# Kernel tuning notes

Hardware: AMD Instinct MI355X
Metric: run time of the kernel (lower is better)

## Reference

```python
import jax, jax.numpy as jnp
import numpy as np

T1, T2, T3 = 0.05, 0.1, 0.15
EPS = 1e-8  # matches torch cosine_similarity clamp


def _propagate(x, t):
    # GEmbedding: cosine-similarity adjacency  [B,N,F] -> [B,N,N]
    xn = x / jnp.maximum(jnp.linalg.norm(x, axis=-1, keepdims=True), EPS)
    adj = jnp.einsum('bnf,bmf->bnm', xn, xn)
    # F.threshold(adj, t, 0): keep values strictly greater than t
    adj = jnp.where(adj > t, adj, 0.0)
    # GraphAdjNorm: D^{-1/2} A D^{-1/2} via row/col broadcast (same math as
    # the original diag-matmul, without materializing diagonal matrices)
    d = jnp.sum(adj, axis=-1)              # [B,N]
    inv_sqrt = 1.0 / jnp.sqrt(d)           # [B,N]
    adj = adj * inv_sqrt[..., :, None] * inv_sqrt[..., None, :]
    return jnp.einsum('bnm,bmf->bnf', adj, x)


def setup_inputs() -> dict:
    key = jax.random.key(0)
    k1, k2 = jax.random.split(key)
    B, N, F = 8, 2048, 128
    x = jax.random.normal(k1, (B, N, F), dtype=jnp.float32)
    weight = jax.random.normal(k2, (F, F), dtype=jnp.float32) * 0.05
    return {"x": x, "weight": weight}


def reference(x, weight):
    res = x
    h = x
    for t in (T1, T2, T3):
        h = _propagate(h, t)
    h = jax.lax.stop_gradient(h)  # torch.no_grad() block
    return jnp.einsum('bnf,fo->bno', h + res, weight)
```

## Files before the change

### kernel.cpp

```cpp
#include <hip/hip_runtime.h>
#include <hip/hip_bf16.h>
#include <cstdint>

#define BQ 8
#define NQ 2048
#define FQ 128
#define NG (NQ * 16)
#define HSS 256.0f

typedef __attribute__((ext_vector_type(8))) short short8;
typedef __attribute__((ext_vector_type(4))) float f32x4;
typedef __attribute__((ext_vector_type(8))) unsigned short us8;
typedef __attribute__((ext_vector_type(2))) unsigned int u32x2;
typedef __attribute__((ext_vector_type(4))) unsigned int u32x4;

__device__ __forceinline__ unsigned short f2bf(float f) {
    union { float f; unsigned int u; } c; c.f = f;
    unsigned int u = c.u;
    u = (u + 0x7FFFu + ((u >> 16) & 1u)) >> 16;
    return (unsigned short)u;
}
__device__ __forceinline__ float bf2f(unsigned short u) {
    union { unsigned int i; float f; } c; c.i = (unsigned int)u << 16; return c.f;
}
__device__ __forceinline__ unsigned int pk8lo(float a, float b, unsigned int old) {
    return (unsigned int)__builtin_amdgcn_cvt_pk_fp8_f32(a, b, (int)old, false);
}
__device__ __forceinline__ unsigned int pk8hi(float a, float b, unsigned int old) {
    return (unsigned int)__builtin_amdgcn_cvt_pk_fp8_f32(a, b, (int)old, true);
}


__global__ __launch_bounds__(256) void k_rownorm(const float* __restrict__ h,
                                                 unsigned short* __restrict__ xnF) {
    int t = threadIdx.x;
    int rl = t >> 4, j = t & 15;
    size_t row = (size_t)blockIdx.x * 16 + rl;
    const float* hr = h + row * FQ + j * 8;
    float v[8];
    #pragma unroll
    for (int e = 0; e < 8; ++e) v[e] = hr[e];
    float s = 0.f;
    #pragma unroll
    for (int e = 0; e < 8; ++e) s += v[e] * v[e];
    s += __shfl_xor(s, 1, 64);
    s += __shfl_xor(s, 2, 64);
    s += __shfl_xor(s, 4, 64);
    s += __shfl_xor(s, 8, 64);
    float inv = 1.0f / fmaxf(sqrtf(s), 1e-8f);
    us8 u;
    #pragma unroll
    for (int e = 0; e < 8; ++e) u[e] = f2bf(v[e] * inv);
    *(us8*)(xnF + (size_t)blockIdx.x * 2048 + j * 128 + rl * 8) = u;
}

__global__ __launch_bounds__(512) void k_adj(const unsigned short* __restrict__ xnF,
                                             unsigned char* __restrict__ adjF,
                                             float* __restrict__ dpart, float t) {
    __shared__ unsigned short As[16384];
    __shared__ union { unsigned short Bsh[16384];
                       unsigned char  T2[128 * 132]; } ub;
    __shared__ float dsm[2][128];
    __shared__ float csm[2][128];

    int bid = blockIdx.x;
    int bb = bid & 7;
    int pr = bid >> 3;
    int I = 0;
    { int p = pr; while (p >= 16 - I) { p -= 16 - I; ++I; } pr = p; }
    int J = I + pr;

    int tid = threadIdx.x;
    int wid = tid >> 6, lane = tid & 63;
    int wr = wid >> 1, wc = wid & 1;
    int g = lane >> 4, c = lane & 15;

    const unsigned short* xb = xnF + (size_t)bb * NQ * FQ;
    int rowb = I * 128 + wr * 32;
    int colb = J * 128 + wc * 64;

    {
        const unsigned short* srcA = xb + (size_t)(I * 8) * 2048;
        const unsigned short* srcB = xb + (size_t)(J * 8) * 2048;
        #pragma unroll
        for (int it = 0; it < 4; ++it) {
            __builtin_amdgcn_global_load_lds(
                (const __attribute__((address_space(1))) void*)(srcA + (size_t)(it * 512 + tid) * 8),
                (__attribute__((address_space(3))) void*)(As + (it * 512 + wid * 64) * 8),
                16, 0, 0);
            __builtin_amdgcn_global_load_lds(
                (const __attribute__((address_space(1))) void*)(srcB + (size_t)(it * 512 + tid) * 8),
                (__attribute__((address_space(3))) void*)(ub.Bsh + (it * 512 + wid * 64) * 8),
                16, 0, 0);
        }
    }
    __syncthreads();

    short8 a[2][4];
    #pragma unroll
    for (int mi = 0; mi < 2; ++mi)
        #pragma unroll
        for (int ks = 0; ks < 4; ++ks)
            a[mi][ks] = *(const short8*)(As + (wr * 2 + mi) * 2048 + (ks * 4 + g) * 128 + c * 8);

    f32x4 acc[2][4];
    #pragma unroll
    for (int mi = 0; mi < 2; ++mi)
        #pragma unroll
        for (int ni = 0; ni < 4; ++ni) acc[mi][ni] = (f32x4){0.f, 0.f, 0.f, 0.f};

    #pragma unroll
    for (int ni = 0; ni < 4; ++ni) {
        short8 b[4];
        #pragma unroll
        for (int ks = 0; ks < 4; ++ks)
            b[ks] = *(const short8*)(ub.Bsh + (wc * 4 + ni) * 2048 + (ks * 4 + g) * 128 + c * 8);
        #pragma unroll
        for (int mi = 0; mi < 2; ++mi)
            #pragma unroll
            for (int ks = 0; ks < 4; ++ks)
                acc[mi][ni] = __builtin_amdgcn_mfma_f32_16x16x32_bf16(a[mi][ks], b[ks], acc[mi][ni], 0, 0, 0);
    }

    __syncthreads();

    unsigned char* adjb = adjF + (size_t)bb * NQ * NQ;
    float dl[2][4];
    float csl[4] = {0.f, 0.f, 0.f, 0.f};
    #pragma unroll
    for (int mi = 0; mi < 2; ++mi)
        #pragma unroll
        for (int r = 0; r < 4; ++r) dl[mi][r] = 0.f;

    #pragma unroll
    for (int mi = 0; mi < 2; ++mi)
        #pragma unroll
        for (int ni = 0; ni < 4; ++ni) {
            f32x4 v = acc[mi][ni];
            float x0 = (v[0] > t) ? v[0] : 0.0f;
            float x1 = (v[1] > t) ? v[1] : 0.0f;
            float x2 = (v[2] > t) ? v[2] : 0.0f;
            float x3 = (v[3] > t) ? v[3] : 0.0f;
            dl[mi][0] += x0; dl[mi][1] += x1; dl[mi][2] += x2; dl[mi][3] += x3;
            csl[ni] += x0 + x1 + x2 + x3;
            unsigned int u = pk8lo(x0, x1, 0u);
            u = pk8hi(x2, x3, u);
            *(unsigned int*)(adjb + (size_t)((colb >> 4) + ni) * NG
                                  + (size_t)((rowb >> 3) + mi * 2 + (g >> 1)) * 128
                                  + c * 8 + (g & 1) * 4) = u;
            if (I != J) {
                int colL = wc * 64 + ni * 16 + c;
                int rowL = wr * 32 + mi * 16 + g * 4;
                *(unsigned int*)(ub.T2 + colL * 132 + rowL) = u;
            }
        }

    #pragma unroll
    for (int mi = 0; mi < 2; ++mi)
        #pragma unroll
        for (int r = 0; r < 4; ++r) {
            float s = dl[mi][r];
            s += __shfl_xor(s, 1, 64);
            s += __shfl_xor(s, 2, 64);
            s += __shfl_xor(s, 4, 64);
            s += __shfl_xor(s, 8, 64);
            dl[mi][r] = s;
        }
    if (c == 0) {
        #pragma unroll
        for (int mi = 0; mi < 2; ++mi)
            #pragma unroll
            for (int r = 0; r < 4; ++r)
                dsm[wc][wr * 32 + mi * 16 + g * 4 + r] = dl[mi][r];
    }
    if (I != J) {
        #pragma unroll
        for (int ni = 0; ni < 4; ++ni) {
            float s = csl[ni];
            s += __shfl_xor(s, 16, 64);
            s += __shfl_xor(s, 32, 64);
            csl[ni] = s;
        }
        if (lane < 16) {
            #pragma unroll
            for (int ni = 0; ni < 4; ++ni)
                csm[wr & 1][wc * 64 + ni * 16 + lane] = csl[ni];
        }
    }
    __syncthreads();
    if (I != J && (wr >= 2) && lane < 16) {
        #pragma unroll
        for (int ni = 0; ni < 4; ++ni)
            csm[wr & 1][wc * 64 + ni * 16 + lane] += csl[ni];
    }
    __syncthreads();

    if (tid < 128)
        dpart[((size_t)J * 8 + bb) * NQ + I * 128 + tid] = dsm[0][tid] + dsm[1][tid];
    if (I != J) {
        if (tid < 128)
            dpart[((size_t)I * 8 + bb) * NQ + J * 128 + tid] = csm[0][tid] + csm[1][tid];
        int ng = wid;
        int mg = lane >> 2;
        int part = lane & 3;
        unsigned int w[8];
        #pragma unroll
        for (int ml = 0; ml < 8; ++ml)
            w[ml] = *(const unsigned int*)(ub.T2 + (mg * 8 + ml) * 132 + ng * 16 + part * 4);
        unsigned int o32[8];
        #pragma unroll
        for (int i = 0; i < 4; ++i)
            #pragma unroll
            for (int h = 0; h < 2; ++h)
                o32[i * 2 + h] = ((w[h * 4 + 0] >> (8 * i)) & 0xFFu)
                               | (((w[h * 4 + 1] >> (8 * i)) & 0xFFu) << 8)
                               | (((w[h * 4 + 2] >> (8 * i)) & 0xFFu) << 16)
                               | (((w[h * 4 + 3] >> (8 * i)) & 0xFFu) << 24);
        unsigned char* dst = adjb + (size_t)(I * 8 + ng) * NG + (size_t)(J * 16 + mg) * 128 + part * 32;
        *(u32x4*)dst        = (u32x4){o32[0], o32[1], o32[2], o32[3]};
        *(u32x4*)(dst + 16) = (u32x4){o32[4], o32[5], o32[6], o32[7]};
    }
}

__global__ __launch_bounds__(256) void k_prep_f32(const float* __restrict__ h,
                                                  const float* __restrict__ dpart,
                                                  float* __restrict__ isq,
                                                  unsigned char* __restrict__ hsF) {
    __shared__ float tile[32][129];
    __shared__ float iv[32];
    int r0 = blockIdx.x * 32;
    int bb = r0 >> 11;
    int m0 = r0 & (NQ - 1);
    int tid = threadIdx.x;
    if (tid < 32) {
        float s = 0.f;
        #pragma unroll
        for (int j = 0; j < 16; ++j)
            s += dpart[((size_t)j * 8 + bb) * NQ + m0 + tid];
        float v = 1.0f / sqrtf(s);
        iv[tid] = v;
        isq[r0 + tid] = v;
    }
    #pragma unroll
    for (int it = 0; it < 16; ++it) {
        int idx = tid + it * 256;
        int mi = idx >> 7, f = idx & 127;
        tile[mi][f] = h[(size_t)(r0 + mi) * FQ + f];
    }
    __syncthreads();
    unsigned char* hb = hsF + (size_t)bb * NQ * FQ;
    #pragma unroll
    for (int it = 0; it < 2; ++it) {
        int p = tid + it * 256;
        int f = p & 127, mc = p >> 7;
        float sv[8];
        #pragma unroll
        for (int e = 0; e < 8; ++e)
            sv[e] = tile[mc * 8 + e][f] * iv[mc * 8 + e] * HSS;
        u32x2 u;
        u[0] = pk8hi(sv[2], sv[3], pk8lo(sv[0], sv[1], 0u));
        u[1] = pk8hi(sv[6], sv[7], pk8lo(sv[4], sv[5], 0u));
        *(u32x2*)(hb + (size_t)((m0 >> 3) + mc) * 1024 + f * 8) = u;
    }
}

__global__ __launch_bounds__(256) void k_prep_bf16(const unsigned short* __restrict__ h,
                                                   const float* __restrict__ dpart,
                                                   float* __restrict__ isq,
                                                   unsigned char* __restrict__ hsF) {
    __shared__ float tile[32][129];
    __shared__ float iv[32];
    int r0 = blockIdx.x * 32;
    int bb = r0 >> 11;
    int m0 = r0 & (NQ - 1);
    int tid = threadIdx.x;
    if (tid < 32) {
        float s = 0.f;
        #pragma unroll
        for (int j = 0; j < 16; ++j)
            s += dpart[((size_t)j * 8 + bb) * NQ + m0 + tid];
        float v = 1.0f / sqrtf(s);
        iv[tid] = v;
        isq[r0 + tid] = v;
    }
    #pragma unroll
    for (int it = 0; it < 16; ++it) {
        int idx = tid + it * 256;
        int mi = idx >> 7, f = idx & 127;
        tile[mi][f] = bf2f(h[(size_t)(r0 + mi) * FQ + f]);
    }
    __syncthreads();
    unsigned char* hb = hsF + (size_t)bb * NQ * FQ;
    #pragma unroll
    for (int it = 0; it < 2; ++it) {
        int p = tid + it * 256;
        int f = p & 127, mc = p >> 7;
        float sv[8];
        #pragma unroll
        for (int e = 0; e < 8; ++e)
            sv[e] = tile[mc * 8 + e][f] * iv[mc * 8 + e] * HSS;
        u32x2 u;
        u[0] = pk8hi(sv[2], sv[3], pk8lo(sv[0], sv[1], 0u));
        u[1] = pk8hi(sv[6], sv[7], pk8lo(sv[4], sv[5], 0u));
        *(u32x2*)(hb + (size_t)((m0 >> 3) + mc) * 1024 + f * 8) = u;
    }
}

template<bool LAST>
__global__ __launch_bounds__(512) void k_gemm3(const unsigned char* __restrict__ adjF,
                                               const unsigned char* __restrict__ hsF,
                                               const float* __restrict__ isq,
                                               unsigned short* __restrict__ hout,
                                               unsigned short* __restrict__ xnF) {
    __shared__ unsigned char Bs[32768];
    __shared__ float red[32][128];

    int bid = blockIdx.x;
    int lb = (bid & 7) * 64 + (bid >> 3);
    int bb = lb >> 6;
    int rt = lb & 63;
    int row0g = rt * 32;
    int tid = threadIdx.x;
    int wid = tid >> 6, lane = tid & 63;
    int g = lane >> 4, c = lane & 15;
    int rg = wid >> 2, kh = wid & 3;
    int wrow = row0g + rg * 16;

    const unsigned char* adjr = adjF + (size_t)bb * NQ * NQ + (size_t)(wrow >> 4) * NG;
    const unsigned char* hb   = hsF + (size_t)bb * NQ * FQ;

    f32x4 acc[8];
    #pragma unroll
    for (int i = 0; i < 8; ++i) acc[i] = (f32x4){0.f, 0.f, 0.f, 0.f};

    int khr = wid >> 1;
    int wlo = wid & 1;

    for (int ph = 0; ph < 8; ++ph) {
        __syncthreads();
        {
            const unsigned char* src = hb + (size_t)(khr * 64 + ph * 8) * 1024 + wlo * 1024;
            unsigned char* dst = Bs + khr * 8192 + wlo * 1024;
            #pragma unroll
            for (int it = 0; it < 4; ++it) {
                __builtin_amdgcn_global_load_lds(
                    (const __attribute__((address_space(1))) void*)(src + it * 2048 + lane * 16),
                    (__attribute__((address_space(3))) void*)(dst + it * 2048),
                    16, 0, 0);
            }
        }
        __syncthreads();
        #pragma unroll
        for (int kk2 = 0; kk2 < 2; ++kk2) {
            int mstep = kh * 16 + ph * 2 + kk2;
            long a0 = *(const long*)(adjr + (size_t)(mstep * 4 + g) * 128 + c * 8);
            #pragma unroll
            for (int ct = 0; ct < 8; ++ct) {
                long bfr = *(const long*)(Bs + kh * 8192 + kk2 * 4096 + g * 1024 + (ct * 16 + c) * 8);
                acc[ct] = __builtin_amdgcn_mfma_f32_16x16x32_fp8_fp8(a0, bfr, acc[ct], 0, 0, 0);
            }
        }
    }

    __syncthreads();
    #pragma unroll
    for (int s = 0; s < 4; ++s) {
        if (kh == s) {
            #pragma unroll
            for (int ct = 0; ct < 8; ++ct)
                #pragma unroll
                for (int r = 0; r < 4; ++r) {
                    int rl = rg * 16 + g * 4 + r;
                    if (s == 0) red[rl][ct * 16 + c] = acc[ct][r];
                    else        red[rl][ct * 16 + c] += acc[ct][r];
                }
        }
        __syncthreads();
    }

    int rl = tid >> 4;
    int j  = tid & 15;
    int n  = row0g + rl;
    float scale = isq[(size_t)bb * NQ + n] * (1.0f / HSS);
    float v[8];
    float s = 0.f;
    #pragma unroll
    for (int e = 0; e < 8; ++e) {
        float x = red[rl][j * 8 + e] * scale;
        v[e] = x;
        s += x * x;
    }
    s += __shfl_xor(s, 1, 64);
    s += __shfl_xor(s, 2, 64);
    s += __shfl_xor(s, 4, 64);
    s += __shfl_xor(s, 8, 64);
    float inv = 1.0f / fmaxf(sqrtf(s), 1e-8f);

    us8 h0;
    #pragma unroll
    for (int e = 0; e < 8; ++e) h0[e] = f2bf(v[e]);
    *(us8*)(hout + ((size_t)bb * NQ + n) * FQ + j * 8) = h0;

    if constexpr (!LAST) {
        us8 u0;
        #pragma unroll
        for (int e = 0; e < 8; ++e) u0[e] = f2bf(v[e] * inv);
        unsigned short* xd = xnF + (size_t)bb * NQ * FQ + (size_t)(n >> 4) * 2048
                                 + j * 128 + (n & 15) * 8;
        *(us8*)xd = u0;
    }
}

__global__ __launch_bounds__(256) void k_out(const unsigned short* __restrict__ h3,
                                             const float* __restrict__ x,
                                             const float* __restrict__ W,
                                             float* __restrict__ out) {
    __shared__ float hx[8][128];
    int r0 = blockIdx.x * 8;
    int tid = threadIdx.x;
    #pragma unroll
    for (int it = 0; it < 4; ++it) {
        int idx = tid + it * 256;
        int ri = idx >> 7, f = idx & 127;
        size_t gi = (size_t)(r0 + ri) * FQ + f;
        hx[ri][f] = bf2f(h3[gi]) + x[gi];
    }
    __syncthreads();
    int o = tid & 127, half = tid >> 7;
    float acc[4] = {0.f, 0.f, 0.f, 0.f};
    for (int f = 0; f < 128; ++f) {
        float wv = W[f * 128 + o];
        #pragma unroll
        for (int j = 0; j < 4; ++j)
            acc[j] += hx[half * 4 + j][f] * wv;
    }
    #pragma unroll
    for (int j = 0; j < 4; ++j)
        out[(size_t)(r0 + half * 4 + j) * FQ + o] = acc[j];
}

extern "C" void kernel_launch(void* const* d_in, const int* in_sizes, int n_in,
                              void* d_out, int out_size, void* d_ws, size_t ws_size,
                              hipStream_t stream) {
    const float* x = (const float*)d_in[0];
    const float* W = (const float*)d_in[1];
    float* out = (float*)d_out;
    char* ws = (char*)d_ws;

    const size_t CS   = (size_t)BQ * NQ * FQ;
    const size_t oADJ = 0;
    const size_t oXN  = oADJ + (size_t)BQ * NQ * NQ;
    const size_t oHST = oXN  + CS * 2;
    const size_t oD   = oHST + CS;
    const size_t oISQ = oD   + (size_t)16 * BQ * NQ * 4;
    const size_t oHA  = oISQ + (size_t)BQ * NQ * 4;
    const size_t oHB  = oHA  + CS * 2;
    const size_t need = oHB  + CS * 2;
    if (ws_size < need) return;

    unsigned char*  adjF = (unsigned char*)(ws + oADJ);
    unsigned short* xnF  = (unsigned short*)(ws + oXN);
    unsigned char*  hsF  = (unsigned char*)(ws + oHST);
    float* dpart = (float*)(ws + oD);
    float* isq   = (float*)(ws + oISQ);
    unsigned short* hA = (unsigned short*)(ws + oHA);
    unsigned short* hB = (unsigned short*)(ws + oHB);

    const float ts[3] = {0.05f, 0.1f, 0.15f};

    k_rownorm<<<BQ * NQ / 16, 256, 0, stream>>>(x, xnF);
    k_adj<<<BQ * 136, 512, 0, stream>>>(xnF, adjF, dpart, ts[0]);
    k_prep_f32<<<BQ * NQ / 32, 256, 0, stream>>>(x, dpart, isq, hsF);
    k_gemm3<false><<<BQ * 64, 512, 0, stream>>>(adjF, hsF, isq, hA, xnF);
    k_adj<<<BQ * 136, 512, 0, stream>>>(xnF, adjF, dpart, ts[1]);
    k_prep_bf16<<<BQ * NQ / 32, 256, 0, stream>>>(hA, dpart, isq, hsF);
    k_gemm3<false><<<BQ * 64, 512, 0, stream>>>(adjF, hsF, isq, hB, xnF);
    k_adj<<<BQ * 136, 512, 0, stream>>>(xnF, adjF, dpart, ts[2]);
    k_prep_bf16<<<BQ * NQ / 32, 256, 0, stream>>>(hB, dpart, isq, hsF);
    k_gemm3<true><<<BQ * 64, 512, 0, stream>>>(adjF, hsF, isq, hA, xnF);

    k_out<<<BQ * NQ / 8, 256, 0, stream>>>(hA, x, W, out);
}
```

Measured before the change: 134.9 us.

## Fuse final residual add and weight projection into last gemm3 via bf16 MFMA

Removes the separate k_out kernel. The last propagation GEMM now adds the residual x and multiplies by W directly from shared memory, using bf16 MFMA with a pre-converted bf16 W layout built by a small new k_wprep kernel. This drops the h3 round trip through global memory, one launch, and the scalar FP32 GEMM loop in k_out. In exchange W and the h+res sum are rounded to bf16, which adds precision error, and there is an extra tiny launch.

```diff
diff --git a/kernel.cpp b/kernel.cpp
--- a/kernel.cpp
+++ b/kernel.cpp
@@ -30,6 +30,19 @@
     return (unsigned int)__builtin_amdgcn_cvt_pk_fp8_f32(a, b, (int)old, true);
 }
 
+
+__global__ __launch_bounds__(256) void k_wprep(const float* __restrict__ W,
+                                               unsigned short* __restrict__ WF) {
+    int b = blockIdx.x;
+    int t = threadIdx.x;
+    int c2 = t & 15;
+    int fc = t >> 4;
+    us8 u;
+    #pragma unroll
+    for (int e = 0; e < 8; ++e)
+        u[e] = f2bf(W[(size_t)(fc * 8 + e) * FQ + b * 16 + c2]);
+    *(us8*)(WF + b * 2048 + fc * 128 + c2 * 8) = u;
+}
 
 __global__ __launch_bounds__(256) void k_rownorm(const float* __restrict__ h,
                                                  unsigned short* __restrict__ xnF) {
@@ -311,7 +324,10 @@
                                                const unsigned char* __restrict__ hsF,
                                                const float* __restrict__ isq,
                                                unsigned short* __restrict__ hout,
-                                               unsigned short* __restrict__ xnF) {
+                                               unsigned short* __restrict__ xnF,
+                                               const unsigned short* __restrict__ WF,
+                                               const float* __restrict__ x,
+                                               float* __restrict__ out) {
     __shared__ unsigned char Bs[32768];
     __shared__ float red[32][128];
 
@@ -378,65 +394,76 @@
         __syncthreads();
     }
 
-    int rl = tid >> 4;
-    int j  = tid & 15;
-    int n  = row0g + rl;
-    float scale = isq[(size_t)bb * NQ + n] * (1.0f / HSS);
-    float v[8];
-    float s = 0.f;
-    #pragma unroll
-    for (int e = 0; e < 8; ++e) {
-        float x = red[rl][j * 8 + e] * scale;
-        v[e] = x;
-        s += x * x;
-    }
-    s += __shfl_xor(s, 1, 64);
-    s += __shfl_xor(s, 2, 64);
-    s += __shfl_xor(s, 4, 64);
-    s += __shfl_xor(s, 8, 64);
-    float inv = 1.0f / fmaxf(sqrtf(s), 1e-8f);
-
-    us8 h0;
-    #pragma unroll
-    for (int e = 0; e < 8; ++e) h0[e] = f2bf(v[e]);
-    *(us8*)(hout + ((size_t)bb * NQ + n) * FQ + j * 8) = h0;
-
     if constexpr (!LAST) {
+        int rl = tid >> 4;
+        int j  = tid & 15;
+        int n  = row0g + rl;
+        float scale = isq[(size_t)bb * NQ + n] * (1.0f / HSS);
+        float v[8];
+        float s = 0.f;
+        #pragma unroll
+        for (int e = 0; e < 8; ++e) {
+            float xv = red[rl][j * 8 + e] * scale;
+            v[e] = xv;
+            s += xv * xv;
+        }
+        s += __shfl_xor(s, 1, 64);
+        s += __shfl_xor(s, 2, 64);
+        s += __shfl_xor(s, 4, 64);
+        s += __shfl_xor(s, 8, 64);
+        float inv = 1.0f / fmaxf(sqrtf(s), 1e-8f);
+
+        us8 h0;
+        #pragma unroll
+        for (int e = 0; e < 8; ++e) h0[e] = f2bf(v[e]);
+        *(us8*)(hout + ((size_t)bb * NQ + n) * FQ + j * 8) = h0;
+
         us8 u0;
         #pragma unroll
         for (int e = 0; e < 8; ++e) u0[e] = f2bf(v[e] * inv);
         unsigned short* xd = xnF + (size_t)bb * NQ * FQ + (size_t)(n >> 4) * 2048
                                  + j * 128 + (n & 15) * 8;
         *(us8*)xd = u0;
-    }
-}
-
-__global__ __launch_bounds__(256) void k_out(const unsigned short* __restrict__ h3,
-                                             const float* __restrict__ x,
-                                             const float* __restrict__ W,
-                                             float* __restrict__ out) {
-    __shared__ float hx[8][128];
-    int r0 = blockIdx.x * 8;
-    int tid = threadIdx.x;
-    #pragma unroll
-    for (int it = 0; it < 4; ++it) {
-        int idx = tid + it * 256;
-        int ri = idx >> 7, f = idx & 127;
-        size_t gi = (size_t)(r0 + ri) * FQ + f;
-        hx[ri][f] = bf2f(h3[gi]) + x[gi];
-    }
-    __syncthreads();
-    int o = tid & 127, half = tid >> 7;
-    float acc[4] = {0.f, 0.f, 0.f, 0.f};
-    for (int f = 0; f < 128; ++f) {
-        float wv = W[f * 128 + o];
-        #pragma unroll
-        for (int j = 0; j < 4; ++j)
-            acc[j] += hx[half * 4 + j][f] * wv;
-    }
-    #pragma unroll
-    for (int j = 0; j < 4; ++j)
-        out[(size_t)(r0 + half * 4 + j) * FQ + o] = acc[j];
+    } else {
+        unsigned short* hxs = (unsigned short*)Bs;
+        {
+            int rl = tid >> 4, j = tid & 15;
+            int n = row0g + rl;
+            float scale = isq[(size_t)bb * NQ + n] * (1.0f / HSS);
+            const float* xr = x + ((size_t)bb * NQ + n) * FQ + j * 8;
+            us8 hxv;
+            #pragma unroll
+            for (int e = 0; e < 8; ++e)
+                hxv[e] = f2bf(red[rl][j * 8 + e] * scale + xr[e]);
+            int wb = (rl * 256 + j * 16) ^ ((rl & 7) << 4);
+            *(us8*)((char*)hxs + wb) = hxv;
+        }
+        __syncthreads();
+        {
+            int rg2 = wid >> 2, oq = wid & 3;
+            f32x4 oacc[2];
+            oacc[0] = (f32x4){0.f, 0.f, 0.f, 0.f};
+            oacc[1] = (f32x4){0.f, 0.f, 0.f, 0.f};
+            int row = rg2 * 16 + c;
+            #pragma unroll
+            for (int ks = 0; ks < 4; ++ks) {
+                short8 af = *(const short8*)((const char*)hxs
+                              + ((row * 256 + ks * 64 + g * 16) ^ ((row & 7) << 4)));
+                #pragma unroll
+                for (int ct = 0; ct < 2; ++ct) {
+                    int og = oq * 2 + ct;
+                    short8 bf = *(const short8*)(WF + og * 2048 + (ks * 4 + g) * 128 + c * 8);
+                    oacc[ct] = __builtin_amdgcn_mfma_f32_16x16x32_bf16(af, bf, oacc[ct], 0, 0, 0);
+                }
+            }
+            float* ob = out + ((size_t)bb * NQ + row0g) * FQ;
+            #pragma unroll
+            for (int ct = 0; ct < 2; ++ct)
+                #pragma unroll
+                for (int r = 0; r < 4; ++r)
+                    ob[(size_t)(rg2 * 16 + g * 4 + r) * FQ + oq * 32 + ct * 16 + c] = oacc[ct][r];
+        }
+    }
 }
 
 extern "C" void kernel_launch(void* const* d_in, const int* in_sizes, int n_in,
@@ -455,7 +482,8 @@
     const size_t oISQ = oD   + (size_t)16 * BQ * NQ * 4;
     const size_t oHA  = oISQ + (size_t)BQ * NQ * 4;
     const size_t oHB  = oHA  + CS * 2;
-    const size_t need = oHB  + CS * 2;
+    const size_t oWF  = oHB  + CS * 2;
+    const size_t need = oWF  + (size_t)FQ * FQ * 2;
     if (ws_size < need) return;
 
     unsigned char*  adjF = (unsigned char*)(ws + oADJ);
@@ -465,19 +493,20 @@
     float* isq   = (float*)(ws + oISQ);
     unsigned short* hA = (unsigned short*)(ws + oHA);
     unsigned short* hB = (unsigned short*)(ws + oHB);
+    unsigned short* WF = (unsigned short*)(ws + oWF);
 
     const float ts[3] = {0.05f, 0.1f, 0.15f};
+
+    k_wprep<<<8, 256, 0, stream>>>(W, WF);
 
     k_rownorm<<<BQ * NQ / 16, 256, 0, stream>>>(x, xnF);
     k_adj<<<BQ * 136, 512, 0, stream>>>(xnF, adjF, dpart, ts[0]);
     k_prep_f32<<<BQ * NQ / 32, 256, 0, stream>>>(x, dpart, isq, hsF);
-    k_gemm3<false><<<BQ * 64, 512, 0, stream>>>(adjF, hsF, isq, hA, xnF);
+    k_gemm3<false><<<BQ * 64, 512, 0, stream>>>(adjF, hsF, isq, hA, xnF, WF, x, out);
     k_adj<<<BQ * 136, 512, 0, stream>>>(xnF, adjF, dpart, ts[1]);
     k_prep_bf16<<<BQ * NQ / 32, 256, 0, stream>>>(hA, dpart, isq, hsF);
-    k_gemm3<false><<<BQ * 64, 512, 0, stream>>>(adjF, hsF, isq, hB, xnF);
+    k_gemm3<false><<<BQ * 64, 512, 0, stream>>>(adjF, hsF, isq, hB, xnF, WF, x, out);
     k_adj<<<BQ * 136, 512, 0, stream>>>(xnF, adjF, dpart, ts[2]);
     k_prep_bf16<<<BQ * NQ / 32, 256, 0, stream>>>(hB, dpart, isq, hsF);
-    k_gemm3<true><<<BQ * 64, 512, 0, stream>>>(adjF, hsF, isq, hA, xnF);
-
-    k_out<<<BQ * NQ / 8, 256, 0, stream>>>(hA, x, W, out);
-}
+    k_gemm3<true><<<BQ * 64, 512, 0, stream>>>(adjF, hsF, isq, hA, xnF, WF, x, out);
+}
```

Result: faster. 122.9 us (-8.9%).
